# Kernel optimization log

Measured on AMD Instinct MI355X. Metric: run time of the kernel, lower is better.

Reference implementation:

```python
import jax, jax.numpy as jnp
import numpy as np

N_NODES = 50000
N_EDGES = 800000
IN_FEATS = 64
OUT_FEATS = 64
EDGE_DIM = 8


def setup_inputs() -> dict:
    key = jax.random.key(0)
    k1, k2, k3, k4, k5 = jax.random.split(key, 5)
    node_feat = jax.random.normal(k1, (N_NODES, IN_FEATS), dtype=jnp.float32)
    edge_feat = jax.random.normal(k2, (N_EDGES, EDGE_DIM), dtype=jnp.float32)
    W = jax.random.normal(k3, (OUT_FEATS, IN_FEATS), dtype=jnp.float32) * (1.0 / np.sqrt(IN_FEATS))
    b = jnp.zeros((OUT_FEATS,), dtype=jnp.float32)
    src = jax.random.randint(k4, (N_EDGES,), 0, N_NODES, dtype=jnp.int64 if jax.config.jax_enable_x64 else jnp.int32)
    dst = jax.random.randint(k5, (N_EDGES,), 0, N_NODES, dtype=jnp.int64 if jax.config.jax_enable_x64 else jnp.int32)
    return {"node_feat": node_feat, "edge_feat": edge_feat, "W": W, "b": b,
            "src": src, "dst": dst}


def reference(node_feat, edge_feat, W, b, src, dst):
    # EfConv forward with aggregate='sum', node_feat.shape[1] == in_feats.
    n_nodes = node_feat.shape[0]
    edge_dim = edge_feat.shape[1]
    h_src = node_feat[src]  # [E, in_feats] gather once, reused for every slice
    aggs = []
    for k in range(edge_dim):  # small fixed loop over edge feature slices
        m = h_src * edge_feat[:, k:k + 1]                      # u_mul_e: [E, in_feats]
        aggs.append(jax.ops.segment_sum(m, dst, num_segments=n_nodes))
    agg = jnp.stack(aggs, axis=1)                              # [N, edge_dim, in_feats]
    # per-slice shared linear, then concat along feature dim
    out = jnp.einsum('nki,oi->nko', agg, W) + b                # [N, edge_dim, out_feats]
    return out.reshape(n_nodes, edge_dim * W.shape[0])         # [N, edge_dim*out_feats]
```

## Files before the change

kernel.cpp:

```cpp
#include <hip/hip_runtime.h>


#define FEATS 64
#define EDGE_DIM 8

__global__ void __launch_bounds__(256) transform_kernel(
    const float* __restrict__ nf, const float* __restrict__ W,
    float* __restrict__ t, int* __restrict__ deg, int n_nodes)
{
    __shared__ float sWt[FEATS * 65];
    __shared__ float srow[4][FEATS];
    const int tid = threadIdx.x;

    int gid = blockIdx.x * 256 + tid;
    if (gid < n_nodes) deg[gid] = 0;

    #pragma unroll
    for (int base = 0; base < FEATS * FEATS; base += 256) {
        int idx = base + tid;
        int o = idx >> 6;
        int i = idx & 63;
        sWt[i * 65 + o] = W[idx];
    }

    const int r = tid >> 6;
    const int o = tid & 63;
    const int node = blockIdx.x * 4 + r;
    if (node < n_nodes) srow[r][o] = nf[(long)node * FEATS + o];
    __syncthreads();

    if (node >= n_nodes) return;
    float sum = 0.f;
    #pragma unroll
    for (int i = 0; i < FEATS; i++)
        sum += srow[r][i] * sWt[i * 65 + o];
    t[(long)node * FEATS + o] = sum;
}

__global__ void __launch_bounds__(256) hist_kernel(
    const int* __restrict__ dst, int* __restrict__ deg, int n_edges)
{
    int i4 = (blockIdx.x * 256 + threadIdx.x) * 4;
    if (i4 + 3 < n_edges) {
        int4 d = *(const int4*)(dst + i4);
        atomicAdd(&deg[d.x], 1);
        atomicAdd(&deg[d.y], 1);
        atomicAdd(&deg[d.z], 1);
        atomicAdd(&deg[d.w], 1);
    } else {
        for (int e = i4; e < n_edges; ++e) atomicAdd(&deg[dst[e]], 1);
    }
}

__global__ void __launch_bounds__(256) partials_kernel(
    const int* __restrict__ deg, int* __restrict__ partials, int n)
{
    __shared__ int s[256];
    int i = blockIdx.x * 256 + threadIdx.x;
    s[threadIdx.x] = (i < n) ? deg[i] : 0;
    __syncthreads();
    for (int off = 128; off > 0; off >>= 1) {
        if (threadIdx.x < off) s[threadIdx.x] += s[threadIdx.x + off];
        __syncthreads();
    }
    if (threadIdx.x == 0) partials[blockIdx.x] = s[0];
}

__global__ void __launch_bounds__(256) scan_partials_kernel(
    const int* __restrict__ partials, int* __restrict__ pscan, int nb)
{
    __shared__ int s[256];
    int tid = threadIdx.x;
    s[tid] = (tid < nb) ? partials[tid] : 0;
    for (int off = 1; off < 256; off <<= 1) {
        __syncthreads();
        int x = (tid >= off) ? s[tid - off] : 0;
        __syncthreads();
        s[tid] += x;
    }
    __syncthreads();
    pscan[tid] = (tid == 0) ? 0 : s[tid - 1];
}

__global__ void __launch_bounds__(256) scan_addback_kernel(
    const int* __restrict__ deg, const int* __restrict__ pscan,
    int* __restrict__ offsets, int* __restrict__ cursor,
    int n, int n_edges)
{
    __shared__ int s[256];
    int tid = threadIdx.x;
    int i = blockIdx.x * 256 + tid;
    int v = (i < n) ? deg[i] : 0;
    s[tid] = v;
    for (int off = 1; off < 256; off <<= 1) {
        __syncthreads();
        int x = (tid >= off) ? s[tid - off] : 0;
        __syncthreads();
        s[tid] += x;
    }
    __syncthreads();
    if (i < n) {
        int excl = pscan[blockIdx.x] + s[tid] - v;
        offsets[i] = excl;
        cursor[i]  = excl;
    }
    if (blockIdx.x == 0 && tid == 0) offsets[n] = n_edges;
}

__global__ void __launch_bounds__(256) permute_kernel(
    const int* __restrict__ src, const int* __restrict__ dst,
    int* __restrict__ cursor, int2* __restrict__ pairs, int n_edges)
{
    int i4 = (blockIdx.x * 256 + threadIdx.x) * 4;
    if (i4 + 3 < n_edges) {
        int4 s = *(const int4*)(src + i4);
        int4 d = *(const int4*)(dst + i4);
        int p;
        p = atomicAdd(&cursor[d.x], 1); pairs[p] = make_int2(s.x, i4 + 0);
        p = atomicAdd(&cursor[d.y], 1); pairs[p] = make_int2(s.y, i4 + 1);
        p = atomicAdd(&cursor[d.z], 1); pairs[p] = make_int2(s.z, i4 + 2);
        p = atomicAdd(&cursor[d.w], 1); pairs[p] = make_int2(s.w, i4 + 3);
    } else {
        for (int e = i4; e < n_edges; ++e) {
            int p = atomicAdd(&cursor[dst[e]], 1);
            pairs[p] = make_int2(src[e], e);
        }
    }
}

#define FMA8(A0, A1, TV)                                \
    acc[0] += A0.x * TV; acc[1] += A0.y * TV;           \
    acc[2] += A0.z * TV; acc[3] += A0.w * TV;           \
    acc[4] += A1.x * TV; acc[5] += A1.y * TV;           \
    acc[6] += A1.z * TV; acc[7] += A1.w * TV;

__global__ void __launch_bounds__(256) aggregate_kernel(
    const float* __restrict__ t, const float* __restrict__ ef,
    const int2* __restrict__ pairs, const int* __restrict__ offsets,
    const float* __restrict__ b, float* __restrict__ out, int n_nodes)
{
    const int node = __builtin_amdgcn_readfirstlane(
        (int)((blockIdx.x * 256 + threadIdx.x) >> 6));
    const int o = threadIdx.x & 63;
    if (node >= n_nodes) return;

    const int beg = offsets[node];
    const int end = offsets[node + 1];
    float acc[EDGE_DIM];
    #pragma unroll
    for (int k = 0; k < EDGE_DIM; k++) acc[k] = 0.f;

    int j = beg;
    for (; j + 3 < end; j += 4) {
        int2 p0 = pairs[j];
        int2 p1 = pairs[j + 1];
        int2 p2 = pairs[j + 2];
        int2 p3 = pairs[j + 3];
        float tv0 = t[(long)p0.x * FEATS + o];
        float tv1 = t[(long)p1.x * FEATS + o];
        float tv2 = t[(long)p2.x * FEATS + o];
        float tv3 = t[(long)p3.x * FEATS + o];
        const float4* q0 = (const float4*)(ef + (long)p0.y * EDGE_DIM);
        const float4* q1 = (const float4*)(ef + (long)p1.y * EDGE_DIM);
        const float4* q2 = (const float4*)(ef + (long)p2.y * EDGE_DIM);
        const float4* q3 = (const float4*)(ef + (long)p3.y * EDGE_DIM);
        float4 a0 = q0[0], a1 = q0[1];
        float4 b0 = q1[0], b1 = q1[1];
        float4 c0 = q2[0], c1 = q2[1];
        float4 d0 = q3[0], d1 = q3[1];
        FMA8(a0, a1, tv0)
        FMA8(b0, b1, tv1)
        FMA8(c0, c1, tv2)
        FMA8(d0, d1, tv3)
    }
    for (; j < end; ++j) {
        int2 p = pairs[j];
        float tv = t[(long)p.x * FEATS + o];
        const float4* q = (const float4*)(ef + (long)p.y * EDGE_DIM);
        float4 a0 = q[0], a1 = q[1];
        FMA8(a0, a1, tv)
    }

    const float bo = b[o];
    float* op = out + (long)node * (EDGE_DIM * FEATS) + o;
    #pragma unroll
    for (int k = 0; k < EDGE_DIM; k++)
        __builtin_nontemporal_store(acc[k] + bo, op + k * FEATS);
}

extern "C" void kernel_launch(void* const* d_in, const int* in_sizes, int n_in,
                              void* d_out, int out_size, void* d_ws, size_t ws_size,
                              hipStream_t stream) {
    const float* node_feat = (const float*)d_in[0];
    const float* edge_feat = (const float*)d_in[1];
    const float* W         = (const float*)d_in[2];
    const float* b         = (const float*)d_in[3];
    const int*   src       = (const int*)d_in[4];
    const int*   dst       = (const int*)d_in[5];
    float* out = (float*)d_out;

    const int n_nodes = in_sizes[0] / FEATS;
    const int n_edges = in_sizes[4];
    const int nb_nodes = (n_nodes + 255) / 256;
    const int nb_e4    = (n_edges + 1023) / 1024;

    int* w = (int*)d_ws;
    float* t      = (float*)w;
    int* deg      = w + (long)n_nodes * FEATS;
    int* offsets  = deg + n_nodes;
    int* cursor   = offsets + n_nodes + 1;
    int* partials = cursor + n_nodes;
    int* pscan    = partials + 256;
    uintptr_t paddr = (uintptr_t)(pscan + 256);
    paddr = (paddr + 7) & ~(uintptr_t)7;
    int2* pairs   = (int2*)paddr;

    transform_kernel<<<(n_nodes + 3) / 4, 256, 0, stream>>>(node_feat, W, t, deg, n_nodes);
    hist_kernel<<<nb_e4, 256, 0, stream>>>(dst, deg, n_edges);
    partials_kernel<<<nb_nodes, 256, 0, stream>>>(deg, partials, n_nodes);
    scan_partials_kernel<<<1, 256, 0, stream>>>(partials, pscan, nb_nodes);
    scan_addback_kernel<<<nb_nodes, 256, 0, stream>>>(deg, pscan, offsets, cursor,
                                                      n_nodes, n_edges);
    permute_kernel<<<nb_e4, 256, 0, stream>>>(src, dst, cursor, pairs, n_edges);

    const long total_ag = (long)n_nodes * 64;
    aggregate_kernel<<<(int)((total_ag + 255) / 256), 256, 0, stream>>>(
        t, edge_feat, pairs, offsets, b, out, n_nodes);
}
```

Before: 319.8 us.

## Permute edge features into CSR order so aggregation reads them sequentially

During the CSR permutation pass, edge features are now scattered into destination-sorted order alongside the source indices. The aggregation kernel can then read edge features contiguously instead of gathering them by edge id, and it processes 8 edges per iteration with clamped indices. The cost is an extra 25.6MB scattered write in the permute pass plus more workspace, with a fallback to the old pair path when the workspace is too small.

```diff
diff --git a/kernel.cpp b/kernel.cpp
--- a/kernel.cpp
+++ b/kernel.cpp
@@ -107,7 +107,87 @@
     if (blockIdx.x == 0 && tid == 0) offsets[n] = n_edges;
 }
 
-__global__ void __launch_bounds__(256) permute_kernel(
+__global__ void __launch_bounds__(256) permute_ef_kernel(
+    const int* __restrict__ src, const int* __restrict__ dst,
+    const float* __restrict__ ef, int* __restrict__ cursor,
+    int* __restrict__ srcs, float* __restrict__ efs, int n_edges)
+{
+    int i4 = (blockIdx.x * 256 + threadIdx.x) * 4;
+    if (i4 + 3 < n_edges) {
+        int4 s = *(const int4*)(src + i4);
+        int4 d = *(const int4*)(dst + i4);
+        const float4* q = (const float4*)(ef + (long)i4 * EDGE_DIM);
+        int p0 = atomicAdd(&cursor[d.x], 1);
+        int p1 = atomicAdd(&cursor[d.y], 1);
+        int p2 = atomicAdd(&cursor[d.z], 1);
+        int p3 = atomicAdd(&cursor[d.w], 1);
+        float4 e0a = q[0], e0b = q[1], e1a = q[2], e1b = q[3];
+        float4 e2a = q[4], e2b = q[5], e3a = q[6], e3b = q[7];
+        srcs[p0] = s.x; srcs[p1] = s.y; srcs[p2] = s.z; srcs[p3] = s.w;
+        float4* w0 = (float4*)(efs + (long)p0 * EDGE_DIM); w0[0] = e0a; w0[1] = e0b;
+        float4* w1 = (float4*)(efs + (long)p1 * EDGE_DIM); w1[0] = e1a; w1[1] = e1b;
+        float4* w2 = (float4*)(efs + (long)p2 * EDGE_DIM); w2[0] = e2a; w2[1] = e2b;
+        float4* w3 = (float4*)(efs + (long)p3 * EDGE_DIM); w3[0] = e3a; w3[1] = e3b;
+    } else {
+        for (int e = i4; e < n_edges; ++e) {
+            int p = atomicAdd(&cursor[dst[e]], 1);
+            srcs[p] = src[e];
+            const float4* q = (const float4*)(ef + (long)e * EDGE_DIM);
+            float4* wv = (float4*)(efs + (long)p * EDGE_DIM);
+            wv[0] = q[0]; wv[1] = q[1];
+        }
+    }
+}
+
+__global__ void __launch_bounds__(256) aggregate_seq_kernel(
+    const float* __restrict__ t, const float* __restrict__ efs,
+    const int* __restrict__ srcs, const int* __restrict__ offsets,
+    const float* __restrict__ b, float* __restrict__ out, int n_nodes)
+{
+    const int node = __builtin_amdgcn_readfirstlane(
+        (int)((blockIdx.x * 256 + threadIdx.x) >> 6));
+    const int o = threadIdx.x & 63;
+    if (node >= n_nodes) return;
+
+    const int beg = offsets[node];
+    const int end = offsets[node + 1];
+    float acc[EDGE_DIM];
+    #pragma unroll
+    for (int k = 0; k < EDGE_DIM; k++) acc[k] = 0.f;
+
+    if (end > beg) {
+        const int last = end - 1;
+        for (int j = beg; j < end; j += 8) {
+            int sidx[8];
+            #pragma unroll
+            for (int u = 0; u < 8; u++) {
+                int jj = j + u;
+                sidx[u] = srcs[jj <= last ? jj : last];
+            }
+            float tv[8];
+            #pragma unroll
+            for (int u = 0; u < 8; u++)
+                tv[u] = t[(long)sidx[u] * FEATS + o];
+            #pragma unroll
+            for (int u = 0; u < 8; u++) {
+                int jj = j + u;
+                int ej = jj <= last ? jj : last;
+                float tvm = (jj <= last) ? tv[u] : 0.f;
+                #pragma unroll
+                for (int k = 0; k < EDGE_DIM; k++)
+                    acc[k] += efs[(long)ej * EDGE_DIM + k] * tvm;
+            }
+        }
+    }
+
+    const float bo = b[o];
+    float* op = out + (long)node * (EDGE_DIM * FEATS) + o;
+    #pragma unroll
+    for (int k = 0; k < EDGE_DIM; k++)
+        __builtin_nontemporal_store(acc[k] + bo, op + k * FEATS);
+}
+
+__global__ void __launch_bounds__(256) permute_pairs_kernel(
     const int* __restrict__ src, const int* __restrict__ dst,
     int* __restrict__ cursor, int2* __restrict__ pairs, int n_edges)
 {
@@ -134,7 +214,7 @@
     acc[4] += A1.x * TV; acc[5] += A1.y * TV;           \
     acc[6] += A1.z * TV; acc[7] += A1.w * TV;
 
-__global__ void __launch_bounds__(256) aggregate_kernel(
+__global__ void __launch_bounds__(256) aggregate_pairs_kernel(
     const float* __restrict__ t, const float* __restrict__ ef,
     const int2* __restrict__ pairs, const int* __restrict__ offsets,
     const float* __restrict__ b, float* __restrict__ out, int n_nodes)
@@ -211,9 +291,14 @@
     int* cursor   = offsets + n_nodes + 1;
     int* partials = cursor + n_nodes;
     int* pscan    = partials + 256;
-    uintptr_t paddr = (uintptr_t)(pscan + 256);
-    paddr = (paddr + 7) & ~(uintptr_t)7;
-    int2* pairs   = (int2*)paddr;
+    int* tail     = pscan + 256;
+
+    uintptr_t sa = (uintptr_t)tail;
+    int* srcs = (int*)sa;
+    uintptr_t ea = (sa + (size_t)n_edges * 4 + 31) & ~(uintptr_t)31;
+    float* efs = (float*)ea;
+    size_t full_end = (ea - (uintptr_t)d_ws) + (size_t)n_edges * EDGE_DIM * 4;
+    bool use_full = full_end <= ws_size;
 
     transform_kernel<<<(n_nodes + 3) / 4, 256, 0, stream>>>(node_feat, W, t, deg, n_nodes);
     hist_kernel<<<nb_e4, 256, 0, stream>>>(dst, deg, n_edges);
@@ -221,9 +306,20 @@
     scan_partials_kernel<<<1, 256, 0, stream>>>(partials, pscan, nb_nodes);
     scan_addback_kernel<<<nb_nodes, 256, 0, stream>>>(deg, pscan, offsets, cursor,
                                                       n_nodes, n_edges);
-    permute_kernel<<<nb_e4, 256, 0, stream>>>(src, dst, cursor, pairs, n_edges);
 
     const long total_ag = (long)n_nodes * 64;
-    aggregate_kernel<<<(int)((total_ag + 255) / 256), 256, 0, stream>>>(
-        t, edge_feat, pairs, offsets, b, out, n_nodes);
-}
+    const int agg_blocks = (int)((total_ag + 255) / 256);
+
+    if (use_full) {
+        permute_ef_kernel<<<nb_e4, 256, 0, stream>>>(src, dst, edge_feat, cursor,
+                                                     srcs, efs, n_edges);
+        aggregate_seq_kernel<<<agg_blocks, 256, 0, stream>>>(
+            t, efs, srcs, offsets, b, out, n_nodes);
+    } else {
+        uintptr_t paddr = (sa + 7) & ~(uintptr_t)7;
+        int2* pairs = (int2*)paddr;
+        permute_pairs_kernel<<<nb_e4, 256, 0, stream>>>(src, dst, cursor, pairs, n_edges);
+        aggregate_pairs_kernel<<<agg_blocks, 256, 0, stream>>>(
+            t, edge_feat, pairs, offsets, b, out, n_nodes);
+    }
+}
```

After: 285.5 us. 1.12x faster.

## Store transformed features and sorted edge features in fp16, widen aggregation unroll

Applied to the files above, without the earlier changes.

The transformed node features are stored as fp16, and edge features are permuted into dst-sorted order as packed fp16 during the permute pass. This replaces the random ef gather in aggregation with sequential reads. The aggregation loop now batches 16 edges per iteration with clamped indices to raise memory-level parallelism. The cost is extra write traffic in the permute kernel and reduced precision, which risks tolerance failures.

```diff
diff --git a/kernel.cpp b/kernel.cpp
--- a/kernel.cpp
+++ b/kernel.cpp
@@ -4,9 +4,11 @@
 #define FEATS 64
 #define EDGE_DIM 8
 
+typedef _Float16 half8 __attribute__((ext_vector_type(8)));
+
 __global__ void __launch_bounds__(256) transform_kernel(
     const float* __restrict__ nf, const float* __restrict__ W,
-    float* __restrict__ t, int* __restrict__ deg, int n_nodes)
+    _Float16* __restrict__ t, int* __restrict__ deg, int n_nodes)
 {
     __shared__ float sWt[FEATS * 65];
     __shared__ float srow[4][FEATS];
@@ -34,7 +36,7 @@
     #pragma unroll
     for (int i = 0; i < FEATS; i++)
         sum += srow[r][i] * sWt[i * 65 + o];
-    t[(long)node * FEATS + o] = sum;
+    t[(long)node * FEATS + o] = (_Float16)sum;
 }
 
 __global__ void __launch_bounds__(256) hist_kernel(
@@ -107,36 +109,53 @@
     if (blockIdx.x == 0 && tid == 0) offsets[n] = n_edges;
 }
 
-__global__ void __launch_bounds__(256) permute_kernel(
+__global__ void __launch_bounds__(256) permute_ef_kernel(
     const int* __restrict__ src, const int* __restrict__ dst,
-    int* __restrict__ cursor, int2* __restrict__ pairs, int n_edges)
+    const float* __restrict__ ef, int* __restrict__ cursor,
+    int* __restrict__ srcs, half8* __restrict__ efs, int n_edges)
 {
     int i4 = (blockIdx.x * 256 + threadIdx.x) * 4;
     if (i4 + 3 < n_edges) {
         int4 s = *(const int4*)(src + i4);
         int4 d = *(const int4*)(dst + i4);
-        int p;
-        p = atomicAdd(&cursor[d.x], 1); pairs[p] = make_int2(s.x, i4 + 0);
-        p = atomicAdd(&cursor[d.y], 1); pairs[p] = make_int2(s.y, i4 + 1);
-        p = atomicAdd(&cursor[d.z], 1); pairs[p] = make_int2(s.z, i4 + 2);
-        p = atomicAdd(&cursor[d.w], 1); pairs[p] = make_int2(s.w, i4 + 3);
+        const float4* q = (const float4*)(ef + (long)i4 * EDGE_DIM);
+        int p0 = atomicAdd(&cursor[d.x], 1);
+        int p1 = atomicAdd(&cursor[d.y], 1);
+        int p2 = atomicAdd(&cursor[d.z], 1);
+        int p3 = atomicAdd(&cursor[d.w], 1);
+        #pragma unroll
+        for (int u = 0; u < 4; u++) {
+            float4 a = q[2 * u], c = q[2 * u + 1];
+            half8 h;
+            h[0] = (_Float16)a.x; h[1] = (_Float16)a.y;
+            h[2] = (_Float16)a.z; h[3] = (_Float16)a.w;
+            h[4] = (_Float16)c.x; h[5] = (_Float16)c.y;
+            h[6] = (_Float16)c.z; h[7] = (_Float16)c.w;
+            int p = (u == 0) ? p0 : (u == 1) ? p1 : (u == 2) ? p2 : p3;
+            __builtin_nontemporal_store(h, &efs[p]);
+        }
+        __builtin_nontemporal_store(s.x, &srcs[p0]);
+        __builtin_nontemporal_store(s.y, &srcs[p1]);
+        __builtin_nontemporal_store(s.z, &srcs[p2]);
+        __builtin_nontemporal_store(s.w, &srcs[p3]);
     } else {
         for (int e = i4; e < n_edges; ++e) {
             int p = atomicAdd(&cursor[dst[e]], 1);
-            pairs[p] = make_int2(src[e], e);
+            srcs[p] = src[e];
+            const float* q = ef + (long)e * EDGE_DIM;
+            half8 h;
+            #pragma unroll
+            for (int k = 0; k < EDGE_DIM; k++) h[k] = (_Float16)q[k];
+            efs[p] = h;
         }
     }
 }
 
-#define FMA8(A0, A1, TV)                                \
-    acc[0] += A0.x * TV; acc[1] += A0.y * TV;           \
-    acc[2] += A0.z * TV; acc[3] += A0.w * TV;           \
-    acc[4] += A1.x * TV; acc[5] += A1.y * TV;           \
-    acc[6] += A1.z * TV; acc[7] += A1.w * TV;
-
-__global__ void __launch_bounds__(256) aggregate_kernel(
-    const float* __restrict__ t, const float* __restrict__ ef,
-    const int2* __restrict__ pairs, const int* __restrict__ offsets,
+#define CHUNK 16
+
+__global__ void __launch_bounds__(256) aggregate_seq_kernel(
+    const _Float16* __restrict__ t, const half8* __restrict__ efs,
+    const int* __restrict__ srcs, const int* __restrict__ offsets,
     const float* __restrict__ b, float* __restrict__ out, int n_nodes)
 {
     const int node = __builtin_amdgcn_readfirstlane(
@@ -150,35 +169,30 @@
     #pragma unroll
     for (int k = 0; k < EDGE_DIM; k++) acc[k] = 0.f;
 
-    int j = beg;
-    for (; j + 3 < end; j += 4) {
-        int2 p0 = pairs[j];
-        int2 p1 = pairs[j + 1];
-        int2 p2 = pairs[j + 2];
-        int2 p3 = pairs[j + 3];
-        float tv0 = t[(long)p0.x * FEATS + o];
-        float tv1 = t[(long)p1.x * FEATS + o];
-        float tv2 = t[(long)p2.x * FEATS + o];
-        float tv3 = t[(long)p3.x * FEATS + o];
-        const float4* q0 = (const float4*)(ef + (long)p0.y * EDGE_DIM);
-        const float4* q1 = (const float4*)(ef + (long)p1.y * EDGE_DIM);
-        const float4* q2 = (const float4*)(ef + (long)p2.y * EDGE_DIM);
-        const float4* q3 = (const float4*)(ef + (long)p3.y * EDGE_DIM);
-        float4 a0 = q0[0], a1 = q0[1];
-        float4 b0 = q1[0], b1 = q1[1];
-        float4 c0 = q2[0], c1 = q2[1];
-        float4 d0 = q3[0], d1 = q3[1];
-        FMA8(a0, a1, tv0)
-        FMA8(b0, b1, tv1)
-        FMA8(c0, c1, tv2)
-        FMA8(d0, d1, tv3)
-    }
-    for (; j < end; ++j) {
-        int2 p = pairs[j];
-        float tv = t[(long)p.x * FEATS + o];
-        const float4* q = (const float4*)(ef + (long)p.y * EDGE_DIM);
-        float4 a0 = q[0], a1 = q[1];
-        FMA8(a0, a1, tv)
+    if (end > beg) {
+        const int last = end - 1;
+        for (int j = beg; j < end; j += CHUNK) {
+            int sidx[CHUNK];
+            #pragma unroll
+            for (int u = 0; u < CHUNK; u++) {
+                int jj = j + u;
+                sidx[u] = srcs[jj <= last ? jj : last];
+            }
+            float tv[CHUNK];
+            #pragma unroll
+            for (int u = 0; u < CHUNK; u++)
+                tv[u] = (float)t[(long)sidx[u] * FEATS + o];
+            #pragma unroll
+            for (int u = 0; u < CHUNK; u++) {
+                int jj = j + u;
+                int ej = jj <= last ? jj : last;
+                float tvm = (jj <= last) ? tv[u] : 0.f;
+                half8 row = efs[ej];
+                #pragma unroll
+                for (int k = 0; k < EDGE_DIM; k++)
+                    acc[k] += (float)row[k] * tvm;
+            }
+        }
     }
 
     const float bo = b[o];
@@ -205,15 +219,15 @@
     const int nb_e4    = (n_edges + 1023) / 1024;
 
     int* w = (int*)d_ws;
-    float* t      = (float*)w;
-    int* deg      = w + (long)n_nodes * FEATS;
+    _Float16* t   = (_Float16*)w;
+    int* deg      = w + (long)n_nodes * (FEATS / 2);
     int* offsets  = deg + n_nodes;
     int* cursor   = offsets + n_nodes + 1;
     int* partials = cursor + n_nodes;
     int* pscan    = partials + 256;
-    uintptr_t paddr = (uintptr_t)(pscan + 256);
-    paddr = (paddr + 7) & ~(uintptr_t)7;
-    int2* pairs   = (int2*)paddr;
+    int* srcs     = pscan + 256;
+    uintptr_t ea  = ((uintptr_t)(srcs + n_edges) + 15) & ~(uintptr_t)15;
+    half8* efs    = (half8*)ea;
 
     transform_kernel<<<(n_nodes + 3) / 4, 256, 0, stream>>>(node_feat, W, t, deg, n_nodes);
     hist_kernel<<<nb_e4, 256, 0, stream>>>(dst, deg, n_edges);
@@ -221,9 +235,10 @@
     scan_partials_kernel<<<1, 256, 0, stream>>>(partials, pscan, nb_nodes);
     scan_addback_kernel<<<nb_nodes, 256, 0, stream>>>(deg, pscan, offsets, cursor,
                                                       n_nodes, n_edges);
-    permute_kernel<<<nb_e4, 256, 0, stream>>>(src, dst, cursor, pairs, n_edges);
+    permute_ef_kernel<<<nb_e4, 256, 0, stream>>>(src, dst, edge_feat, cursor,
+                                                 srcs, efs, n_edges);
 
     const long total_ag = (long)n_nodes * 64;
-    aggregate_kernel<<<(int)((total_ag + 255) / 256), 256, 0, stream>>>(
-        t, edge_feat, pairs, offsets, b, out, n_nodes);
-}
+    aggregate_seq_kernel<<<(int)((total_ag + 255) / 256), 256, 0, stream>>>(
+        t, efs, srcs, offsets, b, out, n_nodes);
+}
```

New measurement: 336.2 us. 5.2% more time.
